# Kernel optimization log

Measured on AMD Instinct MI355X. Metric: run time of the kernel, lower is better.

The kernel has to match this reference:

```python
import jax, jax.numpy as jnp
import numpy as np

B, M, D, Q, H = 16, 4096, 1024, 64, 16
HD = D // H
RESIDUAL_SCALE = 0.1
LN_EPS = 1e-5


def _slot_mask():
    # masked_partition=None default: split slot indices evenly across queries
    mask = np.zeros((Q, M), dtype=bool)
    for qi, chunk in enumerate(np.array_split(np.arange(M), Q)):
        if chunk.size == 0:
            mask[qi, min(qi, M - 1)] = True
        else:
            mask[qi, chunk] = True
    return jnp.asarray(mask)

SLOT_MASK = _slot_mask()  # [Q, M] bool


def setup_inputs() -> dict:
    key = jax.random.key(0)
    ks = jax.random.split(key, 12)
    s = 0.02
    return {
        "memory": jax.random.normal(ks[0], (B, M, D), jnp.float32),
        "context": jax.random.normal(ks[1], (B, D), jnp.float32),
        "memory_mask": jnp.ones((B, M), dtype=bool),
        "queries": jax.random.normal(ks[2], (Q, D), jnp.float32) * s,
        "in_proj_w": jax.random.normal(ks[3], (3 * D, D), jnp.float32) * s,
        "in_proj_b": jnp.zeros((3 * D,), jnp.float32),
        "out_proj_w": jax.random.normal(ks[4], (D, D), jnp.float32) * s,
        "out_proj_b": jnp.zeros((D,), jnp.float32),
        "ctx_w": jax.random.normal(ks[5], (D, D), jnp.float32) * s,
        "ctx_b": jnp.zeros((D,), jnp.float32),
        "ln_g": jnp.ones((D,), jnp.float32),
        "ln_b": jnp.zeros((D,), jnp.float32),
        "gate_w": jax.random.normal(ks[6], (Q, D), jnp.float32) * s,
        "gate_b": jnp.zeros((Q,), jnp.float32),
    }


def _safe_softmax(logits, valid):
    neg = jnp.float32(-jnp.inf)
    ml = jnp.where(valid, logits, neg)
    no_valid = ~jnp.any(valid, axis=-1, keepdims=True)
    ml = jnp.where(no_valid, 0.0, ml)
    w = jax.nn.softmax(ml, axis=-1)
    w = jnp.where(valid, w, 0.0)
    norm = jnp.sum(w, axis=-1, keepdims=True)
    return jnp.where(norm > 0, w / jnp.maximum(norm, 1e-9), 0.0)


def _forward(memory, context, memory_mask, queries, in_proj_w, in_proj_b,
             out_proj_w, out_proj_b, ctx_w, ctx_b, ln_g, ln_b, gate_w, gate_b):
    # conditioning: q = learned queries + projected pooled context ('add')
    cond = context @ ctx_w.T + ctx_b                      # [B, D]
    q = queries[None, :, :] + cond[:, None, :]            # [B, Q, D]

    qw, kw, vw = jnp.split(in_proj_w, 3, axis=0)
    qb, kb, vb = jnp.split(in_proj_b, 3, axis=0)
    pq = (q @ qw.T + qb).reshape(B, Q, H, HD).transpose(0, 2, 1, 3)       # bhqd
    pk = (memory @ kw.T + kb).reshape(B, M, H, HD).transpose(0, 2, 1, 3)  # bhmd
    pv = (memory @ vw.T + vb).reshape(B, M, H, HD).transpose(0, 2, 1, 3)  # bhmd

    logits = jnp.einsum('bhqd,bhmd->bhqm', pq, pk) * (1.0 / jnp.sqrt(jnp.float32(HD)))
    valid = memory_mask[:, None, None, :] & SLOT_MASK[None, None, :, :]   # [B,H,Q,M] (bcast)
    valid = jnp.broadcast_to(valid, logits.shape)
    weights = _safe_softmax(logits, valid)

    attn = jnp.einsum('bhqm,bhmd->bhqd', weights, pv)
    attn = attn.transpose(0, 2, 1, 3).reshape(B, Q, D)
    out = attn @ out_proj_w.T + out_proj_b

    readout = out + RESIDUAL_SCALE * q
    mu = jnp.mean(readout, axis=-1, keepdims=True)
    var = jnp.var(readout, axis=-1, keepdims=True)
    readout = (readout - mu) * jax.lax.rsqrt(var + LN_EPS) * ln_g + ln_b

    gate = jax.nn.sigmoid(context @ gate_w.T + gate_b)    # [B, Q] learned gating
    return readout * gate[:, :, None]


def reference(memory, context, memory_mask, queries, in_proj_w, in_proj_b,
              out_proj_w, out_proj_b, ctx_w, ctx_b, ln_g, ln_b, gate_w, gate_b):
    return _forward(memory, context, memory_mask, queries, in_proj_w, in_proj_b,
                    out_proj_w, out_proj_b, ctx_w, ctx_b, ln_g, ln_b, gate_w, gate_b)
```

## Files before the change

### kernel.cpp

```cpp
#include <hip/hip_runtime.h>
#include <hip/hip_bf16.h>

#define B_ 16
#define M_ 4096
#define D_ 1024
#define Q_ 64
#define H_ 16
#define HD_ 64
#define BQ_ (B_*Q_)
#define CH_ (M_/Q_)

typedef __attribute__((ext_vector_type(8))) short bf16x8;
typedef __attribute__((ext_vector_type(4))) float f32x4;
typedef __attribute__((ext_vector_type(4))) unsigned short u16x4;

#define SWZ(row) (((((row)&7))<<4) ^ ((((row)>>3)&3)<<5))

__device__ __forceinline__ unsigned short f2bf(float f) {
  union { float f; unsigned u; } v; v.f = f;
  unsigned r = v.u + 0x7fffu + ((v.u >> 16) & 1u);
  return (unsigned short)(r >> 16);
}
__device__ __forceinline__ u16x4 f2bf4(float4 v) {
  u16x4 o; o[0] = f2bf(v.x); o[1] = f2bf(v.y); o[2] = f2bf(v.z); o[3] = f2bf(v.w);
  return o;
}
__device__ __forceinline__ unsigned short f2bfi(float f) {
  __hip_bfloat16 h = __float2bfloat16(f);
  union { __hip_bfloat16 h; unsigned short u; } c; c.h = h;
  return c.u;
}

__global__ void k_prep(const float* __restrict__ context, const float* __restrict__ ctx_w,
                       const float* __restrict__ ctx_b, const float* __restrict__ gate_w,
                       const float* __restrict__ gate_b, const float* __restrict__ in_proj_b,
                       const float* __restrict__ out_proj_w, const float* __restrict__ out_proj_b,
                       const float* __restrict__ in_proj_w,
                       float* __restrict__ cond, float* __restrict__ gate,
                       float* __restrict__ obias2,
                       unsigned short* __restrict__ qwb, unsigned short* __restrict__ vwb,
                       unsigned short* __restrict__ owb, unsigned short* __restrict__ kwt) {
  __shared__ unsigned short tile[64 * 66];
  int bid0 = blockIdx.x, t = threadIdx.x;
  if (bid0 < 288) {
    int o = bid0 * 64 + (t >> 2);
    int p = t & 3;
    const float *xv, *wv; float bias; int kind, outidx;
    if (o < B_ * D_) {
      int b = o >> 10, d = o & 1023;
      xv = context + (size_t)b * D_; wv = ctx_w + (size_t)d * D_; bias = ctx_b[d];
      kind = 0; outidx = o;
    } else if (o < B_ * D_ + BQ_) {
      int idx = o - B_ * D_; int b = idx >> 6, qi = idx & 63;
      xv = context + (size_t)b * D_; wv = gate_w + (size_t)qi * D_; bias = gate_b[qi];
      kind = 1; outidx = idx;
    } else {
      int n = o - (B_ * D_ + BQ_);
      xv = in_proj_b + 2 * D_; wv = out_proj_w + (size_t)n * D_; bias = out_proj_b[n];
      kind = 2; outidx = n;
    }
    float s = 0.f;
    #pragma unroll 8
    for (int i = 0; i < 64; ++i) {
      float4 a = ((const float4*)xv)[p + 4 * i];
      float4 c = ((const float4*)wv)[p + 4 * i];
      s += a.x * c.x + a.y * c.y + a.z * c.z + a.w * c.w;
    }
    s += __shfl_xor(s, 1);
    s += __shfl_xor(s, 2);
    s += bias;
    if (p == 0) {
      if (kind == 0) cond[outidx] = s;
      else if (kind == 1) gate[outidx] = 1.f / (1.f + __expf(-s));
      else obias2[outidx] = s;
    }
    return;
  }
  int bid = bid0 - 288;
  if (bid < 3072) {
    int seg = bid >> 10;
    int idx4 = (bid & 1023) * 256 + t;
    float4 v;
    unsigned short* dst;
    if (seg == 0)      { v = ((const float4*)in_proj_w)[idx4];           dst = qwb; }
    else if (seg == 1) { v = ((const float4*)in_proj_w)[524288 + idx4];  dst = vwb; }
    else               { v = ((const float4*)out_proj_w)[idx4];          dst = owb; }
    *(u16x4*)(dst + (size_t)idx4 * 4) = f2bf4(v);
    return;
  }
  int x = bid - 3072;
  int h = x >> 4, db = x & 15;
  #pragma unroll
  for (int rep = 0; rep < 4; ++rep) {
    int e = rep * 16 + (t >> 4), c4 = t & 15;
    float4 v = *(const float4*)(in_proj_w + (size_t)(D_ + h * 64 + e) * D_ + db * 64 + c4 * 4);
    tile[(c4 * 4 + 0) * 66 + e] = f2bf(v.x);
    tile[(c4 * 4 + 1) * 66 + e] = f2bf(v.y);
    tile[(c4 * 4 + 2) * 66 + e] = f2bf(v.z);
    tile[(c4 * 4 + 3) * 66 + e] = f2bf(v.w);
  }
  __syncthreads();
  int dd = t >> 2, e0 = (t & 3) * 16;
  unsigned short* outp = kwt + (size_t)h * 65536 + (size_t)(db * 64 + dd) * 64 + e0;
  #pragma unroll
  for (int u = 0; u < 4; ++u) {
    u16x4 o;
    o[0] = tile[dd * 66 + e0 + u * 4 + 0];
    o[1] = tile[dd * 66 + e0 + u * 4 + 1];
    o[2] = tile[dd * 66 + e0 + u * 4 + 2];
    o[3] = tile[dd * 66 + e0 + u * 4 + 3];
    *(u16x4*)(outp + u * 4) = o;
  }
}

__device__ __forceinline__ void wave_gemm_16x64(const unsigned short* __restrict__ Abase, int lda,
                                                const unsigned short* __restrict__ Bbase, int ldb,
                                                int K, f32x4 acc[4]) {
  const int lane = threadIdx.x & 63;
  const int r = lane & 15, kg = lane >> 4;
  const unsigned short* Ap = Abase + (size_t)r * lda + kg * 8;
  const unsigned short* Bp = Bbase + (size_t)r * ldb + kg * 8;
  #pragma unroll 2
  for (int k0 = 0; k0 < K; k0 += 32) {
    bf16x8 a = *(const bf16x8*)(Ap + k0);
    #pragma unroll
    for (int nt = 0; nt < 4; ++nt) {
      bf16x8 b = *(const bf16x8*)(Bp + (size_t)nt * 16 * ldb + k0);
      acc[nt] = __builtin_amdgcn_mfma_f32_16x16x32_bf16(a, b, acc[nt], 0, 0, 0);
    }
  }
}

__global__ __launch_bounds__(256) void k_qkf(const float* __restrict__ queries,
                                             const float* __restrict__ cond,
                                             const unsigned short* __restrict__ qwb,
                                             const unsigned short* __restrict__ kwt,
                                             const float* __restrict__ ipb,
                                             unsigned short* __restrict__ qk) {
  __shared__ unsigned short pqt[64 * 64];
  const int wv = threadIdx.x >> 6, lane = threadIdx.x & 63, r = lane & 15, kg = lane >> 4;
  const int mt = blockIdx.x, h = blockIdx.y;

  {
    int mr = mt * 64 + wv * 16 + r;
    const float* qrow = queries + (size_t)(mr & 63) * D_;
    const float* crow = cond + (size_t)(mr >> 6) * D_;
    f32x4 acc[4] = {};
    #pragma unroll 2
    for (int k0 = 0; k0 < D_; k0 += 32) {
      int kb = k0 + kg * 8;
      float4 qa0 = *(const float4*)(qrow + kb), qa1 = *(const float4*)(qrow + kb + 4);
      float4 ca0 = *(const float4*)(crow + kb), ca1 = *(const float4*)(crow + kb + 4);
      bf16x8 a;
      a[0] = (short)f2bf(qa0.x + ca0.x); a[1] = (short)f2bf(qa0.y + ca0.y);
      a[2] = (short)f2bf(qa0.z + ca0.z); a[3] = (short)f2bf(qa0.w + ca0.w);
      a[4] = (short)f2bf(qa1.x + ca1.x); a[5] = (short)f2bf(qa1.y + ca1.y);
      a[6] = (short)f2bf(qa1.z + ca1.z); a[7] = (short)f2bf(qa1.w + ca1.w);
      #pragma unroll
      for (int nt = 0; nt < 4; ++nt) {
        bf16x8 b = *(const bf16x8*)(qwb + (size_t)(h * 64 + nt * 16 + r) * D_ + kb);
        acc[nt] = __builtin_amdgcn_mfma_f32_16x16x32_bf16(a, b, acc[nt], 0, 0, 0);
      }
    }
    #pragma unroll
    for (int nt = 0; nt < 4; ++nt)
      #pragma unroll
      for (int j = 0; j < 4; ++j) {
        int row = wv * 16 + kg * 4 + j, col = nt * 16 + r;
        float v = 0.125f * (acc[nt][j] + ipb[h * 64 + col]);
        *(unsigned short*)((char*)pqt + row * 128 + ((col * 2) ^ ((row & 7) << 4))) = f2bf(v);
      }
  }
  __syncthreads();

  {
    bf16x8 bfr[4][2];
    #pragma unroll
    for (int nt = 0; nt < 4; ++nt)
      #pragma unroll
      for (int ks = 0; ks < 2; ++ks) {
        int row = nt * 16 + r, k = ks * 32 + kg * 8;
        bfr[nt][ks] = *(const bf16x8*)((char*)pqt + row * 128 + ((k * 2) ^ ((r & 7) << 4)));
      }
    const unsigned short* kwh = kwt + (size_t)h * 65536;
    #pragma unroll 4
    for (int dt = 0; dt < 16; ++dt) {
      int d0 = wv * 256 + dt * 16;
      bf16x8 a0 = *(const bf16x8*)(kwh + (size_t)(d0 + r) * 64 + kg * 8);
      bf16x8 a1 = *(const bf16x8*)(kwh + (size_t)(d0 + r) * 64 + 32 + kg * 8);
      #pragma unroll
      for (int nt = 0; nt < 4; ++nt) {
        f32x4 acc = {};
        acc = __builtin_amdgcn_mfma_f32_16x16x32_bf16(a0, bfr[nt][0], acc, 0, 0, 0);
        acc = __builtin_amdgcn_mfma_f32_16x16x32_bf16(a1, bfr[nt][1], acc, 0, 0, 0);
        u16x4 o;
        o[0] = f2bf(acc[0]); o[1] = f2bf(acc[1]); o[2] = f2bf(acc[2]); o[3] = f2bf(acc[3]);
        *(u16x4*)(qk + (size_t)(mt * 64 + nt * 16 + r) * 16384 + (size_t)h * 1024 + d0 + kg * 4) = o;
      }
    }
  }
}

__global__ __launch_bounds__(1024, 4) void k_stageB(const float* __restrict__ memory,
                                                    const unsigned short* __restrict__ qk,
                                                    unsigned short* __restrict__ pooled) {
  extern __shared__ char smem[];
  float* lgb = (float*)(smem + 131072);
  unsigned short* wts = (unsigned short*)(smem + 149504);

  const int t = threadIdx.x;
  const int wave = t >> 6, lane = t & 63, r = lane & 15, kg = lane >> 4;
  const int st = wave & 3, kh = wave >> 2;
  const int bq = blockIdx.x;

  const float* cbase = memory + ((size_t)(bq >> 6) * M_ + (size_t)(bq & 63) * CH_) * D_;
  const unsigned short* qkp = qk + (size_t)bq * 16384 + (size_t)r * 1024 + kh * 256;

  bf16x8 qkr[8];
  #pragma unroll
  for (int ks = 0; ks < 8; ++ks) qkr[ks] = *(const bf16x8*)(qkp + ks * 32 + kg * 8);
  float4 va[16];
  const float* wbase = cbase + (size_t)wave * 4096 + lane * 4;
  #pragma unroll
  for (int i = 0; i < 16; ++i) va[i] = *(const float4*)(wbase + i * 256);

  #pragma unroll
  for (int i = 0; i < 16; ++i) {
    int row = wave * 4 + (i >> 2);
    int colb = (((i & 3) * 256 + lane * 4)) * 2;
    u16x4 o;
    o[0] = f2bfi(va[i].x); o[1] = f2bfi(va[i].y);
    o[2] = f2bfi(va[i].z); o[3] = f2bfi(va[i].w);
    *(u16x4*)(smem + row * 2048 + (colb ^ SWZ(row))) = o;
  }
  __syncthreads();

  {
    const int srow = st * 16 + r;
    const int sw = SWZ(srow);
    f32x4 acc = {};
    #pragma unroll
    for (int ks = 0; ks < 8; ++ks) {
      int ke = kh * 256 + ks * 32 + kg * 8;
      bf16x8 bb = *(const bf16x8*)(smem + srow * 2048 + ((ke * 2) ^ sw));
      acc = __builtin_amdgcn_mfma_f32_16x16x32_bf16(qkr[ks], bb, acc, 0, 0, 0);
    }
    #pragma unroll
    for (int j = 0; j < 4; ++j)
      lgb[kh * 1152 + (kg * 4 + j) * 72 + st * 16 + r] = acc[j];
  }
  __syncthreads();

  {
    int h = wave;
    float v = lgb[h * 72 + lane] + lgb[1152 + h * 72 + lane] +
              lgb[2304 + h * 72 + lane] + lgb[3456 + h * 72 + lane];
    float mx = v;
    #pragma unroll
    for (int o = 32; o; o >>= 1) mx = fmaxf(mx, __shfl_xor(mx, o));
    float p = __expf(v - mx);
    float s = p;
    #pragma unroll
    for (int o = 32; o; o >>= 1) s += __shfl_xor(s, o);
    wts[h * 72 + lane] = f2bf(p / s);
  }
  __syncthreads();

  {
    bf16x8 bw[2];
    #pragma unroll
    for (int kk = 0; kk < 2; ++kk)
      bw[kk] = *(const bf16x8*)((char*)wts + r * 144 + (kk * 32 + kg * 8) * 2);
    unsigned short* pout = pooled + (size_t)bq * 16384;
    #pragma unroll
    for (int it = 0; it < 4; ++it) {
      int d0 = wave * 64 + it * 16;
      f32x4 acc = {};
      #pragma unroll
      for (int kk = 0; kk < 2; ++kk) {
        bf16x8 af;
        #pragma unroll
        for (int j = 0; j < 8; ++j) {
          int slot = kk * 32 + kg * 8 + j;
          af[j] = *(const short*)(smem + slot * 2048 + (((d0 + r) * 2) ^ SWZ(slot)));
        }
        acc = __builtin_amdgcn_mfma_f32_16x16x32_bf16(af, bw[kk], acc, 0, 0, 0);
      }
      u16x4 o;
      o[0] = f2bf(acc[0]); o[1] = f2bf(acc[1]); o[2] = f2bf(acc[2]); o[3] = f2bf(acc[3]);
      *(u16x4*)(pout + (size_t)r * 1024 + d0 + kg * 4) = o;
    }
  }
}

__global__ __launch_bounds__(256) void k_vproj(const unsigned short* __restrict__ pooled,
                                               const unsigned short* __restrict__ vwb,
                                               unsigned short* __restrict__ attn) {
  int wv = threadIdx.x >> 6, lane = threadIdx.x & 63, r = lane & 15, kg = lane >> 4;
  int h = blockIdx.y;
  int m0 = blockIdx.x * 64 + wv * 16;
  f32x4 acc[4] = {};
  wave_gemm_16x64(pooled + (size_t)m0 * 16384 + (size_t)h * 1024, 16384,
                  vwb + (size_t)h * HD_ * D_, D_, D_, acc);
  #pragma unroll
  for (int nt = 0; nt < 4; ++nt)
    #pragma unroll
    for (int j = 0; j < 4; ++j) {
      int m = m0 + kg * 4 + j, np = nt * 16 + r;
      attn[(size_t)m * D_ + h * HD_ + np] = f2bf(acc[nt][j]);
    }
}

__global__ __launch_bounds__(256) void k_out(const unsigned short* __restrict__ attn,
                                             const unsigned short* __restrict__ owb,
                                             const float* __restrict__ obias2,
                                             const float* __restrict__ queries,
                                             const float* __restrict__ cond,
                                             float* __restrict__ readout) {
  int wv = threadIdx.x >> 6, lane = threadIdx.x & 63, r = lane & 15, kg = lane >> 4;
  int m0 = blockIdx.x * 64 + wv * 16, n0 = blockIdx.y * 64;
  f32x4 acc[4] = {};
  wave_gemm_16x64(attn + (size_t)m0 * D_, D_, owb + (size_t)n0 * D_, D_, D_, acc);
  #pragma unroll
  for (int nt = 0; nt < 4; ++nt)
    #pragma unroll
    for (int j = 0; j < 4; ++j) {
      int m = m0 + kg * 4 + j, n = n0 + nt * 16 + r;
      int b = m >> 6, qi = m & 63;
      readout[(size_t)m * D_ + n] =
          acc[nt][j] + obias2[n] + 0.1f * (queries[(size_t)qi * D_ + n] + cond[(size_t)b * D_ + n]);
    }
}

__global__ __launch_bounds__(256) void k_ln_gate(const float* __restrict__ readout,
                                                 const float* __restrict__ ln_g,
                                                 const float* __restrict__ ln_b,
                                                 const float* __restrict__ gate,
                                                 float* __restrict__ out) {
  int m = blockIdx.x, t = threadIdx.x;
  float4 v = ((const float4*)(readout + (size_t)m * D_))[t];
  float s = v.x + v.y + v.z + v.w;
  float sq = v.x*v.x + v.y*v.y + v.z*v.z + v.w*v.w;
  for (int off = 32; off; off >>= 1) { s += __shfl_xor(s, off); sq += __shfl_xor(sq, off); }
  __shared__ float ls[4], lq[4];
  if ((t & 63) == 0) { ls[t >> 6] = s; lq[t >> 6] = sq; }
  __syncthreads();
  s = ls[0] + ls[1] + ls[2] + ls[3];
  sq = lq[0] + lq[1] + lq[2] + lq[3];
  float mean = s * (1.f / D_);
  float var = sq * (1.f / D_) - mean * mean;
  float rstd = rsqrtf(var + 1e-5f);
  float g = gate[m];
  float4 gv = ((const float4*)ln_g)[t];
  float4 bv = ((const float4*)ln_b)[t];
  float4 o;
  o.x = ((v.x - mean) * rstd * gv.x + bv.x) * g;
  o.y = ((v.y - mean) * rstd * gv.y + bv.y) * g;
  o.z = ((v.z - mean) * rstd * gv.z + bv.z) * g;
  o.w = ((v.w - mean) * rstd * gv.w + bv.w) * g;
  ((float4*)(out + (size_t)m * D_))[t] = o;
}

extern "C" void kernel_launch(void* const* d_in, const int* in_sizes, int n_in,
                              void* d_out, int out_size, void* d_ws, size_t ws_size,
                              hipStream_t stream) {
  (void)in_sizes; (void)n_in; (void)out_size; (void)ws_size;
  const float* memory     = (const float*)d_in[0];
  const float* context    = (const float*)d_in[1];
  const float* queries    = (const float*)d_in[3];
  const float* in_proj_w  = (const float*)d_in[4];
  const float* in_proj_b  = (const float*)d_in[5];
  const float* out_proj_w = (const float*)d_in[6];
  const float* out_proj_b = (const float*)d_in[7];
  const float* ctx_w      = (const float*)d_in[8];
  const float* ctx_b      = (const float*)d_in[9];
  const float* ln_g       = (const float*)d_in[10];
  const float* ln_b       = (const float*)d_in[11];
  const float* gate_w     = (const float*)d_in[12];
  const float* gate_b     = (const float*)d_in[13];
  float* out = (float*)d_out;

  char* ws = (char*)d_ws;
  size_t off = 0;
  auto alloc = [&](size_t bytes) { char* p = ws + off; off += (bytes + 255) & ~(size_t)255; return p; };
  float* cond            = (float*)alloc((size_t)B_ * D_ * 4);
  float* gate            = (float*)alloc((size_t)BQ_ * 4);
  float* obias2          = (float*)alloc((size_t)D_ * 4);
  unsigned short* qwb    = (unsigned short*)alloc((size_t)D_ * D_ * 2);
  unsigned short* vwb    = (unsigned short*)alloc((size_t)D_ * D_ * 2);
  unsigned short* owb    = (unsigned short*)alloc((size_t)D_ * D_ * 2);
  unsigned short* kwt    = (unsigned short*)alloc((size_t)H_ * D_ * HD_ * 2);
  unsigned short* qk     = (unsigned short*)alloc((size_t)BQ_ * H_ * D_ * 2);
  unsigned short* pooled = (unsigned short*)alloc((size_t)BQ_ * H_ * D_ * 2);
  unsigned short* attn   = (unsigned short*)alloc((size_t)BQ_ * D_ * 2);
  float* readout         = (float*)alloc((size_t)BQ_ * D_ * 4);

  hipFuncSetAttribute((const void*)k_stageB, hipFuncAttributeMaxDynamicSharedMemorySize, 151808);

  k_prep<<<3616, 256, 0, stream>>>(context, ctx_w, ctx_b, gate_w, gate_b, in_proj_b,
                                   out_proj_w, out_proj_b, in_proj_w,
                                   cond, gate, obias2, qwb, vwb, owb, kwt);
  k_qkf<<<dim3(16, 16), 256, 0, stream>>>(queries, cond, qwb, kwt, in_proj_b, qk);
  k_stageB<<<1024, 1024, 151808, stream>>>(memory, qk, pooled);
  k_vproj<<<dim3(16, 16), 256, 0, stream>>>(pooled, vwb, attn);
  k_out<<<dim3(16, 16), 256, 0, stream>>>(attn, owb, obias2, queries, cond, readout);
  k_ln_gate<<<1024, 256, 0, stream>>>(readout, ln_g, ln_b, gate, out);
}
```

Before: 187.6 us.

## Make stageB persistent over four chunks with register prefetch of next chunk

The stageB kernel now launches 256 blocks of 512 threads, and each block walks four (batch, query) chunks in sequence instead of handling one chunk per 1024-thread block. The first half of the next chunk's memory tile and its qk fragments are loaded into registers during the current chunk's weighted-sum phase. This is meant to hide global-load latency behind MFMA work. In exchange, only 256 blocks fill the device (about one per CU, since the 151 KB of shared memory allows one block each), there are more barriers per chunk, and register pressure is higher with two 16-entry float4 arrays live at once.

```diff
diff --git a/kernel.cpp b/kernel.cpp
--- a/kernel.cpp
+++ b/kernel.cpp
@@ -201,95 +201,121 @@
   }
 }
 
-__global__ __launch_bounds__(1024, 4) void k_stageB(const float* __restrict__ memory,
-                                                    const unsigned short* __restrict__ qk,
-                                                    unsigned short* __restrict__ pooled) {
+__global__ __launch_bounds__(512) void k_stageB(const float* __restrict__ memory,
+                                                const unsigned short* __restrict__ qk,
+                                                unsigned short* __restrict__ pooled) {
   extern __shared__ char smem[];
   float* lgb = (float*)(smem + 131072);
   unsigned short* wts = (unsigned short*)(smem + 149504);
 
-  const int t = threadIdx.x;
+  const int t = threadIdx.x, w = blockIdx.x;
   const int wave = t >> 6, lane = t & 63, r = lane & 15, kg = lane >> 4;
-  const int st = wave & 3, kh = wave >> 2;
-  const int bq = blockIdx.x;
-
-  const float* cbase = memory + ((size_t)(bq >> 6) * M_ + (size_t)(bq & 63) * CH_) * D_;
-  const unsigned short* qkp = qk + (size_t)bq * 16384 + (size_t)r * 1024 + kh * 256;
-
+  const int sg2 = wave & 1, kq = wave >> 1;
+
+  float4 pf[16];
   bf16x8 qkr[8];
-  #pragma unroll
-  for (int ks = 0; ks < 8; ++ks) qkr[ks] = *(const bf16x8*)(qkp + ks * 32 + kg * 8);
-  float4 va[16];
-  const float* wbase = cbase + (size_t)wave * 4096 + lane * 4;
-  #pragma unroll
-  for (int i = 0; i < 16; ++i) va[i] = *(const float4*)(wbase + i * 256);
-
-  #pragma unroll
-  for (int i = 0; i < 16; ++i) {
-    int row = wave * 4 + (i >> 2);
-    int colb = (((i & 3) * 256 + lane * 4)) * 2;
-    u16x4 o;
-    o[0] = f2bfi(va[i].x); o[1] = f2bfi(va[i].y);
-    o[2] = f2bfi(va[i].z); o[3] = f2bfi(va[i].w);
-    *(u16x4*)(smem + row * 2048 + (colb ^ SWZ(row))) = o;
-  }
-  __syncthreads();
 
   {
-    const int srow = st * 16 + r;
-    const int sw = SWZ(srow);
-    f32x4 acc = {};
-    #pragma unroll
-    for (int ks = 0; ks < 8; ++ks) {
-      int ke = kh * 256 + ks * 32 + kg * 8;
-      bf16x8 bb = *(const bf16x8*)(smem + srow * 2048 + ((ke * 2) ^ sw));
-      acc = __builtin_amdgcn_mfma_f32_16x16x32_bf16(qkr[ks], bb, acc, 0, 0, 0);
-    }
-    #pragma unroll
-    for (int j = 0; j < 4; ++j)
-      lgb[kh * 1152 + (kg * 4 + j) * 72 + st * 16 + r] = acc[j];
-  }
-  __syncthreads();
-
-  {
-    int h = wave;
-    float v = lgb[h * 72 + lane] + lgb[1152 + h * 72 + lane] +
-              lgb[2304 + h * 72 + lane] + lgb[3456 + h * 72 + lane];
-    float mx = v;
-    #pragma unroll
-    for (int o = 32; o; o >>= 1) mx = fmaxf(mx, __shfl_xor(mx, o));
-    float p = __expf(v - mx);
-    float s = p;
-    #pragma unroll
-    for (int o = 32; o; o >>= 1) s += __shfl_xor(s, o);
-    wts[h * 72 + lane] = f2bf(p / s);
-  }
-  __syncthreads();
-
-  {
-    bf16x8 bw[2];
-    #pragma unroll
-    for (int kk = 0; kk < 2; ++kk)
-      bw[kk] = *(const bf16x8*)((char*)wts + r * 144 + (kk * 32 + kg * 8) * 2);
-    unsigned short* pout = pooled + (size_t)bq * 16384;
-    #pragma unroll
-    for (int it = 0; it < 4; ++it) {
-      int d0 = wave * 64 + it * 16;
+    const float* c0 = memory + (size_t)(4 * w) * 65536;
+    const unsigned short* q0 = qk + (size_t)(4 * w) * 16384 + (size_t)r * 1024;
+    #pragma unroll
+    for (int ks = 0; ks < 8; ++ks) qkr[ks] = *(const bf16x8*)(q0 + kq * 256 + ks * 32 + kg * 8);
+    #pragma unroll
+    for (int i = 0; i < 16; ++i) pf[i] = *(const float4*)(c0 + (size_t)(i * 512 + t) * 4);
+  }
+
+  for (int c = 0; c < 4; ++c) {
+    const int bq = 4 * w + c;
+    {
+      const float* cb = memory + (size_t)bq * 65536;
+      float4 h1[16];
+      #pragma unroll
+      for (int i = 0; i < 16; ++i) h1[i] = *(const float4*)(cb + 32768 + (size_t)(i * 512 + t) * 4);
+      #pragma unroll
+      for (int i = 0; i < 16; ++i) {
+        int idx = i * 512 + t, row = idx >> 8, colb = (idx & 255) * 8;
+        u16x4 o; o[0] = f2bfi(pf[i].x); o[1] = f2bfi(pf[i].y);
+        o[2] = f2bfi(pf[i].z); o[3] = f2bfi(pf[i].w);
+        *(u16x4*)(smem + row * 2048 + (colb ^ SWZ(row))) = o;
+      }
+      #pragma unroll
+      for (int i = 0; i < 16; ++i) {
+        int idx = i * 512 + t, row = 32 + (idx >> 8), colb = (idx & 255) * 8;
+        u16x4 o; o[0] = f2bfi(h1[i].x); o[1] = f2bfi(h1[i].y);
+        o[2] = f2bfi(h1[i].z); o[3] = f2bfi(h1[i].w);
+        *(u16x4*)(smem + row * 2048 + (colb ^ SWZ(row))) = o;
+      }
+    }
+    __syncthreads();
+
+    #pragma unroll
+    for (int g = 0; g < 2; ++g) {
+      const int srow = (sg2 * 2 + g) * 16 + r;
+      const int sw = SWZ(srow);
       f32x4 acc = {};
       #pragma unroll
-      for (int kk = 0; kk < 2; ++kk) {
-        bf16x8 af;
+      for (int ks = 0; ks < 8; ++ks) {
+        int ke = kq * 256 + ks * 32 + kg * 8;
+        bf16x8 bb = *(const bf16x8*)(smem + srow * 2048 + ((ke * 2) ^ sw));
+        acc = __builtin_amdgcn_mfma_f32_16x16x32_bf16(qkr[ks], bb, acc, 0, 0, 0);
+      }
+      #pragma unroll
+      for (int j = 0; j < 4; ++j)
+        lgb[kq * 1152 + (kg * 4 + j) * 72 + (sg2 * 2 + g) * 16 + r] = acc[j];
+    }
+    __syncthreads();
+
+    #pragma unroll
+    for (int hh = 0; hh < 2; ++hh) {
+      int h = wave * 2 + hh;
+      float v = lgb[h * 72 + lane] + lgb[1152 + h * 72 + lane] +
+                lgb[2304 + h * 72 + lane] + lgb[3456 + h * 72 + lane];
+      float mx = v;
+      #pragma unroll
+      for (int o = 32; o; o >>= 1) mx = fmaxf(mx, __shfl_xor(mx, o));
+      float p = __expf(v - mx);
+      float s = p;
+      #pragma unroll
+      for (int o = 32; o; o >>= 1) s += __shfl_xor(s, o);
+      wts[h * 72 + lane] = f2bf(p / s);
+    }
+    __syncthreads();
+
+    if (c < 3) {
+      const float* cn = memory + (size_t)(bq + 1) * 65536;
+      const unsigned short* qn = qk + (size_t)(bq + 1) * 16384 + (size_t)r * 1024;
+      #pragma unroll
+      for (int ks = 0; ks < 8; ++ks) qkr[ks] = *(const bf16x8*)(qn + kq * 256 + ks * 32 + kg * 8);
+      #pragma unroll
+      for (int i = 0; i < 16; ++i) pf[i] = *(const float4*)(cn + (size_t)(i * 512 + t) * 4);
+    }
+
+    {
+      bf16x8 bw[2];
+      #pragma unroll
+      for (int kk = 0; kk < 2; ++kk)
+        bw[kk] = *(const bf16x8*)((char*)wts + r * 144 + (kk * 32 + kg * 8) * 2);
+      unsigned short* pout = pooled + (size_t)bq * 16384;
+      #pragma unroll
+      for (int it = 0; it < 8; ++it) {
+        int d0 = wave * 128 + it * 16;
+        f32x4 acc = {};
         #pragma unroll
-        for (int j = 0; j < 8; ++j) {
-          int slot = kk * 32 + kg * 8 + j;
-          af[j] = *(const short*)(smem + slot * 2048 + (((d0 + r) * 2) ^ SWZ(slot)));
+        for (int kk = 0; kk < 2; ++kk) {
+          bf16x8 af;
+          #pragma unroll
+          for (int j = 0; j < 8; ++j) {
+            int slot = kk * 32 + kg * 8 + j;
+            af[j] = *(const short*)(smem + slot * 2048 + (((d0 + r) * 2) ^ SWZ(slot)));
+          }
+          acc = __builtin_amdgcn_mfma_f32_16x16x32_bf16(af, bw[kk], acc, 0, 0, 0);
         }
-        acc = __builtin_amdgcn_mfma_f32_16x16x32_bf16(af, bw[kk], acc, 0, 0, 0);
-      }
-      u16x4 o;
-      o[0] = f2bf(acc[0]); o[1] = f2bf(acc[1]); o[2] = f2bf(acc[2]); o[3] = f2bf(acc[3]);
-      *(u16x4*)(pout + (size_t)r * 1024 + d0 + kg * 4) = o;
-    }
+        u16x4 o;
+        o[0] = f2bf(acc[0]); o[1] = f2bf(acc[1]); o[2] = f2bf(acc[2]); o[3] = f2bf(acc[3]);
+        *(u16x4*)(pout + (size_t)r * 1024 + d0 + kg * 4) = o;
+      }
+    }
+    __syncthreads();
   }
 }
 
@@ -401,7 +427,7 @@
                                    out_proj_w, out_proj_b, in_proj_w,
                                    cond, gate, obias2, qwb, vwb, owb, kwt);
   k_qkf<<<dim3(16, 16), 256, 0, stream>>>(queries, cond, qwb, kwt, in_proj_b, qk);
-  k_stageB<<<1024, 1024, 151808, stream>>>(memory, qk, pooled);
+  k_stageB<<<256, 512, 151808, stream>>>(memory, qk, pooled);
   k_vproj<<<dim3(16, 16), 256, 0, stream>>>(pooled, vwb, attn);
   k_out<<<dim3(16, 16), 256, 0, stream>>>(attn, owb, obias2, queries, cond, readout);
   k_ln_gate<<<1024, 256, 0, stream>>>(readout, ln_g, ln_b, gate, out);
```

Result: slower. 222.3 us (+18.5%).

## Make stageB blocks persistent over four chunks with prefetch of next memory chunk

Applied to the files above, without the earlier changes.

Each stageB block now processes four consecutive (batch,query) chunks instead of one, using 256 blocks instead of 1024. While computing the pooled output for the current chunk, it loads the next chunk's fp32 memory into registers and writes it to LDS in halves, overlapping global loads with MFMA work. The cost is more barriers per chunk and fewer blocks on the device. With 256 blocks against a GPU's CU count, and one block per CU given the LDS use, parallelism and latency hiding may suffer.

```diff
diff --git a/kernel.cpp b/kernel.cpp
--- a/kernel.cpp
+++ b/kernel.cpp
@@ -201,95 +201,123 @@
   }
 }
 
-__global__ __launch_bounds__(1024, 4) void k_stageB(const float* __restrict__ memory,
-                                                    const unsigned short* __restrict__ qk,
-                                                    unsigned short* __restrict__ pooled) {
+__global__ __launch_bounds__(1024) void k_stageB(const float* __restrict__ memory,
+                                                 const unsigned short* __restrict__ qk,
+                                                 unsigned short* __restrict__ pooled) {
   extern __shared__ char smem[];
   float* lgb = (float*)(smem + 131072);
   unsigned short* wts = (unsigned short*)(smem + 149504);
 
-  const int t = threadIdx.x;
+  const int t = threadIdx.x, w = blockIdx.x;
   const int wave = t >> 6, lane = t & 63, r = lane & 15, kg = lane >> 4;
   const int st = wave & 3, kh = wave >> 2;
-  const int bq = blockIdx.x;
-
-  const float* cbase = memory + ((size_t)(bq >> 6) * M_ + (size_t)(bq & 63) * CH_) * D_;
-  const unsigned short* qkp = qk + (size_t)bq * 16384 + (size_t)r * 1024 + kh * 256;
-
-  bf16x8 qkr[8];
-  #pragma unroll
-  for (int ks = 0; ks < 8; ++ks) qkr[ks] = *(const bf16x8*)(qkp + ks * 32 + kg * 8);
-  float4 va[16];
-  const float* wbase = cbase + (size_t)wave * 4096 + lane * 4;
-  #pragma unroll
-  for (int i = 0; i < 16; ++i) va[i] = *(const float4*)(wbase + i * 256);
-
-  #pragma unroll
-  for (int i = 0; i < 16; ++i) {
-    int row = wave * 4 + (i >> 2);
-    int colb = (((i & 3) * 256 + lane * 4)) * 2;
-    u16x4 o;
-    o[0] = f2bfi(va[i].x); o[1] = f2bfi(va[i].y);
-    o[2] = f2bfi(va[i].z); o[3] = f2bfi(va[i].w);
-    *(u16x4*)(smem + row * 2048 + (colb ^ SWZ(row))) = o;
+
+  {
+    const float* cb = memory + (size_t)(4 * w) * 65536;
+    #pragma unroll
+    for (int hf = 0; hf < 2; ++hf) {
+      float4 va[8];
+      #pragma unroll
+      for (int i = 0; i < 8; ++i) {
+        int j = i * 1024 + t;
+        va[i] = *(const float4*)(cb + (size_t)(j >> 7) * 1024 + hf * 512 + (j & 127) * 4);
+      }
+      #pragma unroll
+      for (int i = 0; i < 8; ++i) {
+        int j = i * 1024 + t, row = j >> 7, colb = hf * 1024 + (j & 127) * 8;
+        u16x4 o; o[0] = f2bfi(va[i].x); o[1] = f2bfi(va[i].y);
+        o[2] = f2bfi(va[i].z); o[3] = f2bfi(va[i].w);
+        *(u16x4*)(smem + row * 2048 + (colb ^ SWZ(row))) = o;
+      }
+    }
   }
   __syncthreads();
 
-  {
-    const int srow = st * 16 + r;
-    const int sw = SWZ(srow);
-    f32x4 acc = {};
-    #pragma unroll
-    for (int ks = 0; ks < 8; ++ks) {
-      int ke = kh * 256 + ks * 32 + kg * 8;
-      bf16x8 bb = *(const bf16x8*)(smem + srow * 2048 + ((ke * 2) ^ sw));
-      acc = __builtin_amdgcn_mfma_f32_16x16x32_bf16(qkr[ks], bb, acc, 0, 0, 0);
-    }
-    #pragma unroll
-    for (int j = 0; j < 4; ++j)
-      lgb[kh * 1152 + (kg * 4 + j) * 72 + st * 16 + r] = acc[j];
-  }
-  __syncthreads();
-
-  {
-    int h = wave;
-    float v = lgb[h * 72 + lane] + lgb[1152 + h * 72 + lane] +
-              lgb[2304 + h * 72 + lane] + lgb[3456 + h * 72 + lane];
-    float mx = v;
-    #pragma unroll
-    for (int o = 32; o; o >>= 1) mx = fmaxf(mx, __shfl_xor(mx, o));
-    float p = __expf(v - mx);
-    float s = p;
-    #pragma unroll
-    for (int o = 32; o; o >>= 1) s += __shfl_xor(s, o);
-    wts[h * 72 + lane] = f2bf(p / s);
-  }
-  __syncthreads();
-
-  {
+  for (int c = 0; c < 4; ++c) {
+    const int bq = 4 * w + c;
+
+    {
+      const unsigned short* qkp = qk + (size_t)bq * 16384 + (size_t)r * 1024 + kh * 256;
+      bf16x8 qkr[8];
+      #pragma unroll
+      for (int ks = 0; ks < 8; ++ks) qkr[ks] = *(const bf16x8*)(qkp + ks * 32 + kg * 8);
+      const int srow = st * 16 + r;
+      const int sw = SWZ(srow);
+      f32x4 acc = {};
+      #pragma unroll
+      for (int ks = 0; ks < 8; ++ks) {
+        int ke = kh * 256 + ks * 32 + kg * 8;
+        bf16x8 bb = *(const bf16x8*)(smem + srow * 2048 + ((ke * 2) ^ sw));
+        acc = __builtin_amdgcn_mfma_f32_16x16x32_bf16(qkr[ks], bb, acc, 0, 0, 0);
+      }
+      #pragma unroll
+      for (int j = 0; j < 4; ++j)
+        lgb[kh * 1152 + (kg * 4 + j) * 72 + st * 16 + r] = acc[j];
+    }
+    __syncthreads();
+
+    {
+      int h = wave;
+      float v = lgb[h * 72 + lane] + lgb[1152 + h * 72 + lane] +
+                lgb[2304 + h * 72 + lane] + lgb[3456 + h * 72 + lane];
+      float mx = v;
+      #pragma unroll
+      for (int o = 32; o; o >>= 1) mx = fmaxf(mx, __shfl_xor(mx, o));
+      float p = __expf(v - mx);
+      float s = p;
+      #pragma unroll
+      for (int o = 32; o; o >>= 1) s += __shfl_xor(s, o);
+      wts[h * 72 + lane] = f2bf(p / s);
+    }
+    __syncthreads();
+
     bf16x8 bw[2];
     #pragma unroll
     for (int kk = 0; kk < 2; ++kk)
       bw[kk] = *(const bf16x8*)((char*)wts + r * 144 + (kk * 32 + kg * 8) * 2);
     unsigned short* pout = pooled + (size_t)bq * 16384;
-    #pragma unroll
-    for (int it = 0; it < 4; ++it) {
-      int d0 = wave * 64 + it * 16;
-      f32x4 acc = {};
-      #pragma unroll
-      for (int kk = 0; kk < 2; ++kk) {
-        bf16x8 af;
+    const float* cn = memory + (size_t)(bq + 1) * 65536;
+
+    #pragma unroll
+    for (int hf = 0; hf < 2; ++hf) {
+      float4 va[8];
+      if (c < 3) {
         #pragma unroll
-        for (int j = 0; j < 8; ++j) {
-          int slot = kk * 32 + kg * 8 + j;
-          af[j] = *(const short*)(smem + slot * 2048 + (((d0 + r) * 2) ^ SWZ(slot)));
+        for (int i = 0; i < 8; ++i) {
+          int j = i * 1024 + t;
+          va[i] = *(const float4*)(cn + (size_t)(j >> 7) * 1024 + hf * 512 + (j & 127) * 4);
         }
-        acc = __builtin_amdgcn_mfma_f32_16x16x32_bf16(af, bw[kk], acc, 0, 0, 0);
-      }
-      u16x4 o;
-      o[0] = f2bf(acc[0]); o[1] = f2bf(acc[1]); o[2] = f2bf(acc[2]); o[3] = f2bf(acc[3]);
-      *(u16x4*)(pout + (size_t)r * 1024 + d0 + kg * 4) = o;
-    }
+      }
+      #pragma unroll
+      for (int it = 0; it < 2; ++it) {
+        int d0 = hf * 512 + wave * 32 + it * 16;
+        f32x4 acc = {};
+        #pragma unroll
+        for (int kk = 0; kk < 2; ++kk) {
+          bf16x8 af;
+          #pragma unroll
+          for (int j = 0; j < 8; ++j) {
+            int slot = kk * 32 + kg * 8 + j;
+            af[j] = *(const short*)(smem + slot * 2048 + (((d0 + r) * 2) ^ SWZ(slot)));
+          }
+          acc = __builtin_amdgcn_mfma_f32_16x16x32_bf16(af, bw[kk], acc, 0, 0, 0);
+        }
+        u16x4 o;
+        o[0] = f2bf(acc[0]); o[1] = f2bf(acc[1]); o[2] = f2bf(acc[2]); o[3] = f2bf(acc[3]);
+        *(u16x4*)(pout + (size_t)r * 1024 + d0 + kg * 4) = o;
+      }
+      __syncthreads();
+      if (c < 3) {
+        #pragma unroll
+        for (int i = 0; i < 8; ++i) {
+          int j = i * 1024 + t, row = j >> 7, colb = hf * 1024 + (j & 127) * 8;
+          u16x4 o; o[0] = f2bfi(va[i].x); o[1] = f2bfi(va[i].y);
+          o[2] = f2bfi(va[i].z); o[3] = f2bfi(va[i].w);
+          *(u16x4*)(smem + row * 2048 + (colb ^ SWZ(row))) = o;
+        }
+      }
+    }
+    __syncthreads();
   }
 }
 
@@ -401,7 +429,7 @@
                                    out_proj_w, out_proj_b, in_proj_w,
                                    cond, gate, obias2, qwb, vwb, owb, kwt);
   k_qkf<<<dim3(16, 16), 256, 0, stream>>>(queries, cond, qwb, kwt, in_proj_b, qk);
-  k_stageB<<<1024, 1024, 151808, stream>>>(memory, qk, pooled);
+  k_stageB<<<256, 1024, 151808, stream>>>(memory, qk, pooled);
   k_vproj<<<dim3(16, 16), 256, 0, stream>>>(pooled, vwb, attn);
   k_out<<<dim3(16, 16), 256, 0, stream>>>(attn, owb, obias2, queries, cond, readout);
   k_ln_gate<<<1024, 256, 0, stream>>>(readout, ln_g, ln_b, gate, out);
```

New measurement: 223.5 us. +19.1%, slower.
